# Kernel tuning notes

Measured on AMD Instinct MI355X. Metric: run time of the kernel, lower is better.

Reference implementation:

```python
import jax, jax.numpy as jnp
import numpy as np

S, N, C = 16384, 2048, 8  # n_samples, n_channels, n_components

def setup_inputs() -> dict:
    key = jax.random.key(0)
    k1, k2, k3, k4 = jax.random.split(key, 4)
    return {
        "inputs": jax.random.uniform(k1, (S, N), dtype=jnp.float32),
        "components": jax.random.uniform(k2, (C, N), dtype=jnp.float32),
        "contributions": jax.random.uniform(k3, (S, C), dtype=jnp.float32),
        "shift": jax.random.normal(k4, (S, C), dtype=jnp.float32) * 3.0,
    }

def reference(inputs, components, contributions, shift):
    # fit_shift=True branch. The original builds k_matrix[i,j] = j - i and
    # coeff[i,j] = clip(1 - |shift - (j - i)|, 0, 1), then dots with the
    # component. That is exactly linear interpolation of component at
    # position i + shift, with zero padding outside [0, N-1].
    n_samples, n_channels = inputs.shape
    n_comp = components.shape[0]
    i = jnp.arange(n_channels, dtype=shift.dtype)
    pos = i[None, None, :] + shift[:, :, None]            # [S, C, N]
    j0f = jnp.floor(pos)
    frac = pos - j0f                                      # in [0, 1)
    j0 = j0f.astype(jnp.int32)
    j1 = j0 + 1
    cidx = jnp.arange(n_comp)[None, :, None]              # broadcast over [S, C, N]
    g0 = components[cidx, jnp.clip(j0, 0, n_channels - 1)]
    g1 = components[cidx, jnp.clip(j1, 0, n_channels - 1)]
    v0 = ((j0 >= 0) & (j0 < n_channels)).astype(components.dtype)
    v1 = ((j1 >= 0) & (j1 < n_channels)).astype(components.dtype)
    shifted = g0 * (1.0 - frac) * v0 + g1 * frac * v1     # [S, C, N] shifted components
    # scale by per-sample contributions and sum over components
    return jnp.einsum('scn,sc->sn', shifted, contributions)
```

## Files before the change

kernel.cpp:

```cpp
#include <hip/hip_runtime.h>
#include <hip/hip_fp16.h>


namespace {
constexpr int kS     = 16384;
constexpr int kN     = 2048;
constexpr int kC     = 8;
constexpr int kM     = 16;
constexpr int kBlock = 512;
constexpr int kPadH  = 32;
constexpr int kUnits = 1057;
constexpr int kRowStride = 1192;

__device__ __forceinline__ int swz(int u) { return u + (u >> 3); }

__global__ __launch_bounds__(kBlock, 8)
void smf_kernel(const float* __restrict__ comps,
                const float* __restrict__ contrib,
                const float* __restrict__ shift,
                float* __restrict__ out)
{
    __shared__ uint32_t ldsU[kC * kRowStride];
    __shared__ float    ctLds[kM * kC];
    __shared__ float    shLds[kM * kC];

    const int tid = threadIdx.x;
    const int s0  = blockIdx.x * kM;

    for (int c = 0; c < kC; ++c) {
        const float* src = comps + c * kN;
        uint32_t* dst = ldsU + c * kRowStride;
        for (int u = tid; u < kUnits; u += kBlock) {
            const int j = 2 * u - kPadH;
            float2 v = make_float2(0.f, 0.f);
            if (j >= 0 && j < kN - 1) v = *reinterpret_cast<const float2*>(src + j);
            __half2 h2 = __floats2half2_rn(v.x, v.y);
            dst[swz(u)] = *reinterpret_cast<const uint32_t*>(&h2);
        }
    }

    for (int tt = tid; tt < (kM * kC) / 2; tt += kBlock) {
        if (tt < (kM * kC) / 4) {
            reinterpret_cast<float4*>(ctLds)[tt] =
                reinterpret_cast<const float4*>(contrib + (size_t)s0 * kC)[tt];
        } else {
            const int t2 = tt - (kM * kC) / 4;
            reinterpret_cast<float4*>(shLds)[t2] =
                reinterpret_cast<const float4*>(shift + (size_t)s0 * kC)[t2];
        }
    }
    __syncthreads();

    const int q = tid >> 8;
    const int t = tid & 255;

    #pragma unroll 1
    for (int r = 0; r < kM / 2; ++r) {
        const int si = q * (kM / 2) + r;
        const int s  = s0 + si;

        const float4 ccA = *reinterpret_cast<const float4*>(ctLds + si * kC);
        const float4 ccB = *reinterpret_cast<const float4*>(ctLds + si * kC + 4);
        const float4 csA = *reinterpret_cast<const float4*>(shLds + si * kC);
        const float4 csB = *reinterpret_cast<const float4*>(shLds + si * kC + 4);

        const float ct[8] = {ccA.x, ccA.y, ccA.z, ccA.w, ccB.x, ccB.y, ccB.z, ccB.w};
        const float sh[8] = {csA.x, csA.y, csA.z, csA.w, csB.x, csB.y, csB.z, csB.w};

        float accA[4], accB[4];
        #pragma unroll
        for (int k = 0; k < 4; ++k) { accA[k] = 0.f; accB[k] = 0.f; }

        #pragma unroll
        for (int c = 0; c < kC; ++c) {
            const float fl = floorf(sh[c]);
            const float fr = sh[c] - fl;
            int d = (int)fl;
            d = d < -31 ? -31 : (d > 31 ? 31 : d);
            const float w1 = ct[c] * fr;
            const float w0 = ct[c] - w1;

            const int a   = 4 * t + d + kPadH;
            const int u0  = a >> 1;
            const bool odd = (a & 1) != 0;

            const uint32_t* row = ldsU + c * kRowStride;
            const uint32_t yA0 = row[swz(u0 + 0)];
            const uint32_t yA1 = row[swz(u0 + 1)];
            const uint32_t yA2 = row[swz(u0 + 2)];
            const uint32_t yB0 = row[swz(u0 + 512)];
            const uint32_t yB1 = row[swz(u0 + 513)];
            const uint32_t yB2 = row[swz(u0 + 514)];

            const uint32_t zA0 = odd ? __builtin_amdgcn_alignbit(yA1, yA0, 16) : yA0;
            const uint32_t zA1 = odd ? __builtin_amdgcn_alignbit(yA2, yA1, 16) : yA1;
            const uint32_t zA2 = odd ? (yA2 >> 16) : yA2;
            const uint32_t zB0 = odd ? __builtin_amdgcn_alignbit(yB1, yB0, 16) : yB0;
            const uint32_t zB1 = odd ? __builtin_amdgcn_alignbit(yB2, yB1, 16) : yB1;
            const uint32_t zB2 = odd ? (yB2 >> 16) : yB2;

            const float2 fA0 = __half22float2(*reinterpret_cast<const __half2*>(&zA0));
            const float2 fA1 = __half22float2(*reinterpret_cast<const __half2*>(&zA1));
            const float2 fA2 = __half22float2(*reinterpret_cast<const __half2*>(&zA2));
            const float2 fB0 = __half22float2(*reinterpret_cast<const __half2*>(&zB0));
            const float2 fB1 = __half22float2(*reinterpret_cast<const __half2*>(&zB1));
            const float2 fB2 = __half22float2(*reinterpret_cast<const __half2*>(&zB2));

            accA[0] += w0 * fA0.x + w1 * fA0.y;
            accA[1] += w0 * fA0.y + w1 * fA1.x;
            accA[2] += w0 * fA1.x + w1 * fA1.y;
            accA[3] += w0 * fA1.y + w1 * fA2.x;
            accB[0] += w0 * fB0.x + w1 * fB0.y;
            accB[1] += w0 * fB0.y + w1 * fB1.x;
            accB[2] += w0 * fB1.x + w1 * fB1.y;
            accB[3] += w0 * fB1.y + w1 * fB2.x;
        }

        float* orow = out + (size_t)s * kN;
        *reinterpret_cast<float4*>(orow + 4 * t) =
            make_float4(accA[0], accA[1], accA[2], accA[3]);
        *reinterpret_cast<float4*>(orow + 1024 + 4 * t) =
            make_float4(accB[0], accB[1], accB[2], accB[3]);
    }
}
}

extern "C" void kernel_launch(void* const* d_in, const int* in_sizes, int n_in,
                              void* d_out, int out_size, void* d_ws, size_t ws_size,
                              hipStream_t stream) {
    const float* comps   = (const float*)d_in[1];
    const float* contrib = (const float*)d_in[2];
    const float* shiftp  = (const float*)d_in[3];
    float* out = (float*)d_out;

    dim3 grid(kS / kM);
    dim3 block(kBlock);
    smf_kernel<<<grid, block, 0, stream>>>(comps, contrib, shiftp, out);
}
```

Measured before the change: 285.5 us.

## Recast shifted-component sum as sparse fp16 GEMM on MFMA with workspace buffers

Builds a banded fp16 matrix of shifted component copies (Gt, 35 shift slots per component) and a per-sample sparse weight matrix A, then computes the output as a 16384x320 by 320x2048 MFMA GEMM. The intent is to replace LDS gather and FMA work with matrix-core throughput. It adds three preprocessing kernels and workspace traffic, clamps shifts to [-17,16] where the old path allowed up to ±31, and keeps the old kernel as a fallback when the workspace is too small.

```diff
diff --git a/kernel.cpp b/kernel.cpp
--- a/kernel.cpp
+++ b/kernel.cpp
@@ -3,48 +3,208 @@
 
 
 namespace {
-constexpr int kS     = 16384;
-constexpr int kN     = 2048;
-constexpr int kC     = 8;
-constexpr int kM     = 16;
-constexpr int kBlock = 512;
+constexpr int kS = 16384;
+constexpr int kN = 2048;
+constexpr int kC = 8;
+constexpr int kK = 320;
+constexpr int kSlots = 40;
+constexpr size_t kGtBytes = (size_t)kN * kK * 2;
+constexpr size_t kABytes  = (size_t)kS * kK * 2;
+constexpr size_t kWsNeed  = kGtBytes + kABytes;
+
+typedef _Float16 f16x8 __attribute__((ext_vector_type(8)));
+typedef float    f32x4 __attribute__((ext_vector_type(4)));
+
+__global__ __launch_bounds__(256)
+void zeroA_kernel(uint4* __restrict__ a4) {
+    const int idx = blockIdx.x * 256 + threadIdx.x;
+    const int n4  = (int)(kABytes / 16);
+    if (idx < n4) a4[idx] = make_uint4(0u, 0u, 0u, 0u);
+}
+
+__global__ __launch_bounds__(256)
+void buildG_kernel(const float* __restrict__ comps, __half* __restrict__ Gt) {
+    const int tid = blockIdx.x * 256 + threadIdx.x;
+    const int c = tid >> 11;
+    const int n = tid & 2047;
+    const float* src = comps + c * kN;
+
+    uint32_t w[kSlots / 2];
+    #pragma unroll
+    for (int t2 = 0; t2 < kSlots / 2; ++t2) {
+        uint32_t pk = 0;
+        #pragma unroll
+        for (int h = 0; h < 2; ++h) {
+            const int t = 2 * t2 + h;
+            float v = 0.f;
+            if (t < 35) {
+                const int j = n + (t - 17);
+                if (j >= 0 && j < kN) v = src[j];
+            }
+            const __half hv = __float2half_rn(v);
+            pk |= (uint32_t)__half_as_ushort(hv) << (16 * h);
+        }
+        w[t2] = pk;
+    }
+    uint4* dst = reinterpret_cast<uint4*>(Gt + (size_t)n * kK + c * kSlots);
+    #pragma unroll
+    for (int i = 0; i < kSlots / 8; ++i)
+        dst[i] = make_uint4(w[4 * i], w[4 * i + 1], w[4 * i + 2], w[4 * i + 3]);
+}
+
+__global__ __launch_bounds__(256)
+void buildA_kernel(const float* __restrict__ contrib,
+                   const float* __restrict__ shift,
+                   __half* __restrict__ A) {
+    const int tid = blockIdx.x * 256 + threadIdx.x;
+    const int s = tid >> 3;
+    const int c = tid & 7;
+    const float ctv = contrib[(size_t)s * kC + c];
+    const float sv  = shift[(size_t)s * kC + c];
+    float fl = floorf(sv);
+    int d = (int)fl;
+    d = d < -17 ? -17 : (d > 16 ? 16 : d);
+    const float fr = sv - (float)d;
+    const __half w1h = __float2half_rn(ctv * fr);
+    const __half w0h = __float2half_rn(ctv - __half2float(w1h));
+    __half* row = A + (size_t)s * kK + c * kSlots;
+    row[d + 17] = w0h;
+    row[d + 18] = w1h;
+}
+
+__global__ __launch_bounds__(256, 2)
+void gemm_kernel(const __half* __restrict__ A, const __half* __restrict__ Gt,
+                 float* __restrict__ out) {
+    __shared__ __align__(16) __half At[128 * 64];
+    __shared__ __align__(16) __half Bt[128 * 64];
+
+    const int tid = threadIdx.x;
+    const int bm = blockIdx.x >> 4;
+    const int bn = blockIdx.x & 15;
+    const int s0 = bm * 128, n0 = bn * 128;
+
+    const int rbase = tid >> 3;
+    const int t8    = tid & 7;
+    const __half* srcA[4];
+    const __half* srcB[4];
+    int dst[4];
+    #pragma unroll
+    for (int q = 0; q < 4; ++q) {
+        const int rr = q * 32 + rbase;
+        const int slot = t8 ^ (rr & 7);
+        srcA[q] = A  + (size_t)(s0 + rr) * kK + slot * 8;
+        srcB[q] = Gt + (size_t)(n0 + rr) * kK + slot * 8;
+        dst[q]  = rr * 64 + t8 * 8;
+    }
+
+    const int lane = tid & 63, wave = tid >> 6;
+    const int wm = (wave >> 1) * 64, wn = (wave & 1) * 64;
+    const int l15 = lane & 15, l4 = lane >> 4, p = lane & 7;
+    const int aOff0 = (wm + l15) * 64 + ((l4)     ^ p) * 8;
+    const int aOff1 = (wm + l15) * 64 + ((4 + l4) ^ p) * 8;
+    const int bOff0 = (wn + l15) * 64 + ((l4)     ^ p) * 8;
+    const int bOff1 = (wn + l15) * 64 + ((4 + l4) ^ p) * 8;
+
+    f32x4 acc[4][4];
+    #pragma unroll
+    for (int mi = 0; mi < 4; ++mi)
+        #pragma unroll
+        for (int ni = 0; ni < 4; ++ni)
+            acc[mi][ni] = f32x4{0.f, 0.f, 0.f, 0.f};
+
+    uint4 ta[4], tb[4];
+    #pragma unroll
+    for (int q = 0; q < 4; ++q) {
+        ta[q] = *reinterpret_cast<const uint4*>(srcA[q]);
+        tb[q] = *reinterpret_cast<const uint4*>(srcB[q]);
+    }
+
+    #pragma unroll 1
+    for (int step = 0; step < 5; ++step) {
+        #pragma unroll
+        for (int q = 0; q < 4; ++q) {
+            *reinterpret_cast<uint4*>(&At[dst[q]]) = ta[q];
+            *reinterpret_cast<uint4*>(&Bt[dst[q]]) = tb[q];
+        }
+        __syncthreads();
+        if (step < 4) {
+            #pragma unroll
+            for (int q = 0; q < 4; ++q) {
+                srcA[q] += 64; srcB[q] += 64;
+                ta[q] = *reinterpret_cast<const uint4*>(srcA[q]);
+                tb[q] = *reinterpret_cast<const uint4*>(srcB[q]);
+            }
+        }
+        #pragma unroll
+        for (int ks = 0; ks < 2; ++ks) {
+            const int ao = ks ? aOff1 : aOff0;
+            const int bo = ks ? bOff1 : bOff0;
+            f16x8 af[4], bf[4];
+            #pragma unroll
+            for (int mi = 0; mi < 4; ++mi)
+                af[mi] = *reinterpret_cast<const f16x8*>(&At[ao + mi * 1024]);
+            #pragma unroll
+            for (int ni = 0; ni < 4; ++ni)
+                bf[ni] = *reinterpret_cast<const f16x8*>(&Bt[bo + ni * 1024]);
+            #pragma unroll
+            for (int mi = 0; mi < 4; ++mi)
+                #pragma unroll
+                for (int ni = 0; ni < 4; ++ni)
+                    acc[mi][ni] = __builtin_amdgcn_mfma_f32_16x16x32_f16(
+                        af[mi], bf[ni], acc[mi][ni], 0, 0, 0);
+        }
+        __syncthreads();
+    }
+
+    #pragma unroll
+    for (int mi = 0; mi < 4; ++mi) {
+        #pragma unroll
+        for (int v = 0; v < 4; ++v) {
+            float* orow = out + (size_t)(s0 + wm + mi * 16 + l4 * 4 + v) * kN
+                              + n0 + wn + l15;
+            #pragma unroll
+            for (int ni = 0; ni < 4; ++ni) orow[ni * 16] = acc[mi][ni][v];
+        }
+    }
+}
+
+constexpr int kMf     = 16;
+constexpr int kBlockF = 512;
 constexpr int kPadH  = 32;
 constexpr int kUnits = 1057;
 constexpr int kRowStride = 1192;
-
 __device__ __forceinline__ int swz(int u) { return u + (u >> 3); }
 
-__global__ __launch_bounds__(kBlock, 8)
+__global__ __launch_bounds__(kBlockF, 8)
 void smf_kernel(const float* __restrict__ comps,
                 const float* __restrict__ contrib,
                 const float* __restrict__ shift,
                 float* __restrict__ out)
 {
     __shared__ uint32_t ldsU[kC * kRowStride];
-    __shared__ float    ctLds[kM * kC];
-    __shared__ float    shLds[kM * kC];
+    __shared__ float    ctLds[kMf * kC];
+    __shared__ float    shLds[kMf * kC];
 
     const int tid = threadIdx.x;
-    const int s0  = blockIdx.x * kM;
+    const int s0  = blockIdx.x * kMf;
 
     for (int c = 0; c < kC; ++c) {
         const float* src = comps + c * kN;
-        uint32_t* dst = ldsU + c * kRowStride;
-        for (int u = tid; u < kUnits; u += kBlock) {
+        uint32_t* dstp = ldsU + c * kRowStride;
+        for (int u = tid; u < kUnits; u += kBlockF) {
             const int j = 2 * u - kPadH;
             float2 v = make_float2(0.f, 0.f);
             if (j >= 0 && j < kN - 1) v = *reinterpret_cast<const float2*>(src + j);
             __half2 h2 = __floats2half2_rn(v.x, v.y);
-            dst[swz(u)] = *reinterpret_cast<const uint32_t*>(&h2);
-        }
-    }
-
-    for (int tt = tid; tt < (kM * kC) / 2; tt += kBlock) {
-        if (tt < (kM * kC) / 4) {
+            dstp[swz(u)] = *reinterpret_cast<const uint32_t*>(&h2);
+        }
+    }
+    for (int tt = tid; tt < (kMf * kC) / 2; tt += kBlockF) {
+        if (tt < (kMf * kC) / 4) {
             reinterpret_cast<float4*>(ctLds)[tt] =
                 reinterpret_cast<const float4*>(contrib + (size_t)s0 * kC)[tt];
         } else {
-            const int t2 = tt - (kM * kC) / 4;
+            const int t2 = tt - (kMf * kC) / 4;
             reinterpret_cast<float4*>(shLds)[t2] =
                 reinterpret_cast<const float4*>(shift + (size_t)s0 * kC)[t2];
         }
@@ -55,22 +215,18 @@
     const int t = tid & 255;
 
     #pragma unroll 1
-    for (int r = 0; r < kM / 2; ++r) {
-        const int si = q * (kM / 2) + r;
+    for (int r = 0; r < kMf / 2; ++r) {
+        const int si = q * (kMf / 2) + r;
         const int s  = s0 + si;
-
         const float4 ccA = *reinterpret_cast<const float4*>(ctLds + si * kC);
         const float4 ccB = *reinterpret_cast<const float4*>(ctLds + si * kC + 4);
         const float4 csA = *reinterpret_cast<const float4*>(shLds + si * kC);
         const float4 csB = *reinterpret_cast<const float4*>(shLds + si * kC + 4);
-
         const float ct[8] = {ccA.x, ccA.y, ccA.z, ccA.w, ccB.x, ccB.y, ccB.z, ccB.w};
         const float sh[8] = {csA.x, csA.y, csA.z, csA.w, csB.x, csB.y, csB.z, csB.w};
-
         float accA[4], accB[4];
         #pragma unroll
         for (int k = 0; k < 4; ++k) { accA[k] = 0.f; accB[k] = 0.f; }
-
         #pragma unroll
         for (int c = 0; c < kC; ++c) {
             const float fl = floorf(sh[c]);
@@ -79,11 +235,9 @@
             d = d < -31 ? -31 : (d > 31 ? 31 : d);
             const float w1 = ct[c] * fr;
             const float w0 = ct[c] - w1;
-
             const int a   = 4 * t + d + kPadH;
             const int u0  = a >> 1;
             const bool odd = (a & 1) != 0;
-
             const uint32_t* row = ldsU + c * kRowStride;
             const uint32_t yA0 = row[swz(u0 + 0)];
             const uint32_t yA1 = row[swz(u0 + 1)];
@@ -91,21 +245,18 @@
             const uint32_t yB0 = row[swz(u0 + 512)];
             const uint32_t yB1 = row[swz(u0 + 513)];
             const uint32_t yB2 = row[swz(u0 + 514)];
-
             const uint32_t zA0 = odd ? __builtin_amdgcn_alignbit(yA1, yA0, 16) : yA0;
             const uint32_t zA1 = odd ? __builtin_amdgcn_alignbit(yA2, yA1, 16) : yA1;
             const uint32_t zA2 = odd ? (yA2 >> 16) : yA2;
             const uint32_t zB0 = odd ? __builtin_amdgcn_alignbit(yB1, yB0, 16) : yB0;
             const uint32_t zB1 = odd ? __builtin_amdgcn_alignbit(yB2, yB1, 16) : yB1;
             const uint32_t zB2 = odd ? (yB2 >> 16) : yB2;
-
             const float2 fA0 = __half22float2(*reinterpret_cast<const __half2*>(&zA0));
             const float2 fA1 = __half22float2(*reinterpret_cast<const __half2*>(&zA1));
             const float2 fA2 = __half22float2(*reinterpret_cast<const __half2*>(&zA2));
             const float2 fB0 = __half22float2(*reinterpret_cast<const __half2*>(&zB0));
             const float2 fB1 = __half22float2(*reinterpret_cast<const __half2*>(&zB1));
             const float2 fB2 = __half22float2(*reinterpret_cast<const __half2*>(&zB2));
-
             accA[0] += w0 * fA0.x + w1 * fA0.y;
             accA[1] += w0 * fA0.y + w1 * fA1.x;
             accA[2] += w0 * fA1.x + w1 * fA1.y;
@@ -115,7 +266,6 @@
             accB[2] += w0 * fB1.x + w1 * fB1.y;
             accB[3] += w0 * fB1.y + w1 * fB2.x;
         }
-
         float* orow = out + (size_t)s * kN;
         *reinterpret_cast<float4*>(orow + 4 * t) =
             make_float4(accA[0], accA[1], accA[2], accA[3]);
@@ -133,7 +283,15 @@
     const float* shiftp  = (const float*)d_in[3];
     float* out = (float*)d_out;
 
-    dim3 grid(kS / kM);
-    dim3 block(kBlock);
-    smf_kernel<<<grid, block, 0, stream>>>(comps, contrib, shiftp, out);
-}
+    if (ws_size >= kWsNeed && d_ws != nullptr) {
+        __half* Gt = (__half*)d_ws;
+        __half* A  = (__half*)((char*)d_ws + kGtBytes);
+        zeroA_kernel<<<dim3((int)(kABytes / 16 / 256)), dim3(256), 0, stream>>>(
+            (uint4*)A);
+        buildG_kernel<<<dim3((kC * kN) / 256), dim3(256), 0, stream>>>(comps, Gt);
+        buildA_kernel<<<dim3((kS * kC) / 256), dim3(256), 0, stream>>>(contrib, shiftp, A);
+        gemm_kernel<<<dim3((kS / 128) * (kN / 128)), dim3(256), 0, stream>>>(A, Gt, out);
+    } else {
+        smf_kernel<<<dim3(kS / kMf), dim3(kBlockF), 0, stream>>>(comps, contrib, shiftp, out);
+    }
+}
```

Result: slower. 320.7 us (+12.3%).
